# Performance work log

Measured on AMD Instinct MI355X. Metric: run time of the kernel, lower is better.

Reference implementation:

```python
import jax, jax.numpy as jnp
import numpy as np

IMAGE = 128            # canvas_size == image_size -> resize is identity
N_LINES = 32
N_SEGMENTS = 2
N_POINTS = 5           # control points per line (2 shared-endpoint quadratic beziers)
N_COLOR = 3
COORDPAIRS = np.array([[0, 1, 2], [2, 3, 4]])  # (n_segments, 3)
N_SAMPLES = 10         # polyline samples for bezier edt2 (explicit 10 in source)
POWER = 2.0            # power at progress=0 (= config.power_i)
SIGMA2 = 0.05          # annealed sigma2 at progress=0
EPS = 1e-10
BS = 4


def setup_inputs() -> dict:
    key = jax.random.key(0)
    k1, k2, k3, k4 = jax.random.split(key, 4)
    position = 0.5 * jax.random.normal(k1, (BS, N_LINES, N_POINTS * 2), jnp.float32)
    radius = jax.random.uniform(k2, (BS, N_LINES, 1), jnp.float32, minval=0.3, maxval=1.0)
    color = jax.random.uniform(k3, (BS, N_LINES, N_COLOR), jnp.float32)
    background = jax.random.uniform(k4, (BS, N_COLOR), jnp.float32)
    return {"position": position, "radius": radius, "color": color, "background": background}


def _render(position, radius, color, background):
    bs = position.shape[0]
    r = jnp.linspace(-1.0, 1.0, IMAGE)
    gy, gx = jnp.meshgrid(r, r, indexing="ij")
    grid = jnp.stack([gy, gx], axis=-1)                      # (H, W, 2)

    # --- reshape_params (background='keep', n_back=0) ---
    lines = position.reshape(bs, N_LINES, N_POINTS, 2)
    segs = lines[:, :, COORDPAIRS]                           # (bs, nl, nseg, 3, 2)
    # smooth bezier: reflect control point of segments after the first
    segs = segs.at[:, :, 1:, 1].set(2.0 * segs[:, :, 1:, 0] - segs[:, :, 1:, 1])
    curves = segs.reshape(bs, N_LINES * N_SEGMENTS, 3, 2)    # (bs, N, 3, 2)

    sigma = (radius ** 2).reshape(bs, N_LINES, 1, 1)
    sigma = jnp.repeat(sigma, N_SEGMENTS, axis=1) * SIGMA2   # (bs, N, 1, 1)
    col = jnp.repeat(color, N_SEGMENTS, axis=1)[:, :, :, None, None]  # (bs, N, nc, 1, 1)

    # --- curve_edt2_polyline: sample quadratic bezier, min segment distance ---
    t = jnp.linspace(0.0, 1.0, N_SAMPLES)
    w = jnp.stack([(1.0 - t) ** 2, 2.0 * t * (1.0 - t), t ** 2], axis=0)  # (3, T)
    pts = jnp.einsum("bnkc,kt->bntc", curves, w)             # (bs, N, T, 2)
    a, b = pts[:, :, :-1], pts[:, :, 1:]                     # (bs, N, S=T-1, 2)
    v = b - a
    v_ = v[:, :, :, None, None, :]
    d = grid[None, None, None] - a[:, :, :, None, None, :]   # (bs, N, S, H, W, 2)
    vv = jnp.sum(v * v, axis=-1)[:, :, :, None, None]
    tp = jnp.clip(jnp.sum(d * v_, axis=-1) / (vv + EPS), 0.0, 1.0)
    diff = d - tp[..., None] * v_
    edt2 = jnp.min(jnp.sum(diff * diff, axis=-1), axis=2)    # (bs, N, H, W)

    # --- intensity + rasterize + over-composite ---
    intensity = jnp.exp(-((edt2 / sigma) ** POWER))          # (bs, N, H, W)
    rasters = col * intensity[:, :, None]                    # (bs, N, nc, H, W)
    canvas = jnp.broadcast_to(background[:, None, :, None, None],
                              (bs, 1, N_COLOR, IMAGE, IMAGE))
    rasters = jnp.concatenate([rasters, canvas], axis=1)     # (bs, N+1, nc, H, W)
    inten_c = jnp.broadcast_to(intensity[:, :, None],
                               (bs, intensity.shape[1], N_COLOR, IMAGE, IMAGE))
    inten_all = jnp.concatenate([inten_c, jnp.ones_like(canvas)], axis=1)
    linv = 1.0 - inten_all + EPS
    # 'over' composite front-to-back along stroke dim: exclusive cumprod weights
    w_excl = jnp.concatenate([jnp.ones_like(linv[:, :1]),
                              jnp.cumprod(linv, axis=1)[:, :-1]], axis=1)
    images = jnp.sum(rasters * w_excl, axis=1)               # (bs, nc, H, W)
    return jnp.clip(images, 0.0, 1.0)


def reference(position, radius, color, background):
    return _render(position, radius, color, background)
```

## Files before the change

### kernel.cpp

```cpp
#include <hip/hip_runtime.h>

#define IMAGE   128
#define NLINES  32
#define NCURVE  64
#define NSUB    9
#define PIX     (IMAGE*IMAGE)

__global__ __launch_bounds__(256)
void render_kernel(const float* __restrict__ pos,
                   const float* __restrict__ rad,
                   const float* __restrict__ col,
                   const float* __restrict__ bg,
                   float* __restrict__ out)
{
    __shared__ float4 s_seg[NCURVE*NSUB];
    __shared__ float  s_rvv[NCURVE*NSUB];
    __shared__ float  s_isig[NCURVE];
    __shared__ float  s_col[NCURVE*3];
    __shared__ float  s_bg[3];

    const int tid  = threadIdx.x;
    const int b    = blockIdx.x >> 6;
    const int pblk = blockIdx.x & 63;

    for (int e = tid; e < NCURVE*NSUB; e += 256) {
        const int n    = e / NSUB;
        const int j    = e - n*NSUB;
        const int line = n >> 1;
        const int seg  = n & 1;
        const float* P = pos + (b*NLINES + line)*10;
        float c0x, c0y, c1x, c1y, c2x, c2y;
        if (seg == 0) {
            c0x = P[0]; c0y = P[1];
            c1x = P[2]; c1y = P[3];
            c2x = P[4]; c2y = P[5];
        } else {
            const float q2x = P[4], q2y = P[5];
            const float q3x = P[6], q3y = P[7];
            c0x = q2x;             c0y = q2y;
            c1x = 2.0f*q2x - q3x;  c1y = 2.0f*q2y - q3y;
            c2x = P[8];            c2y = P[9];
        }
        const float t0 = (float)j     * (1.0f/9.0f);
        const float t1 = (float)(j+1) * (1.0f/9.0f);
        float ax, ay, bx, by;
        {
            const float mt = 1.0f - t0;
            const float w0 = mt*mt, w1 = 2.0f*t0*mt, w2 = t0*t0;
            ax = w0*c0x + w1*c1x + w2*c2x;
            ay = w0*c0y + w1*c1y + w2*c2y;
        }
        {
            const float mt = 1.0f - t1;
            const float w0 = mt*mt, w1 = 2.0f*t1*mt, w2 = t1*t1;
            bx = w0*c0x + w1*c1x + w2*c2x;
            by = w0*c0y + w1*c1y + w2*c2y;
        }
        const float vx = bx - ax, vy = by - ay;
        s_seg[e] = make_float4(ax, ay, vx, vy);
        s_rvv[e] = 1.0f / (vx*vx + vy*vy + 1e-10f);
    }
    if (tid < NCURVE) {
        const float r = rad[b*NLINES + (tid >> 1)];
        s_isig[tid] = 1.0f / (r*r*0.05f);
    }
    if (tid < NCURVE*3) {
        const int n = tid/3, c = tid - n*3;
        s_col[tid] = col[(b*NLINES + (n >> 1))*3 + c];
    }
    if (tid < 3) s_bg[tid] = bg[b*3 + tid];
    __syncthreads();

    const int p = pblk*256 + tid;
    const float g0 = -1.0f + (float)(p >> 7)  * (2.0f/127.0f);
    const float g1 = -1.0f + (float)(p & 127) * (2.0f/127.0f);

    float aR = 0.0f, aG = 0.0f, aB = 0.0f, T = 1.0f;
    for (int n = 0; n < NCURVE; ++n) {
        float edt2 = 3.4e38f;
        #pragma unroll
        for (int j = 0; j < NSUB; ++j) {
            const float4 s  = s_seg[n*NSUB + j];
            const float rvv = s_rvv[n*NSUB + j];
            const float d0  = g0 - s.x;
            const float d1  = g1 - s.y;
            const float dt  = d0*s.z + d1*s.w;
            const float tp  = fminf(fmaxf(dt*rvv, 0.0f), 1.0f);
            const float e0  = d0 - tp*s.z;
            const float e1  = d1 - tp*s.w;
            edt2 = fminf(edt2, e0*e0 + e1*e1);
        }
        const float xs = edt2 * s_isig[n];
        const float I  = __expf(-xs*xs);
        const float wI = I * T;
        aR = fmaf(s_col[n*3+0], wI, aR);
        aG = fmaf(s_col[n*3+1], wI, aG);
        aB = fmaf(s_col[n*3+2], wI, aB);
        T *= (1.0f - I + 1e-10f);
    }
    aR = fmaf(s_bg[0], T, aR);
    aG = fmaf(s_bg[1], T, aG);
    aB = fmaf(s_bg[2], T, aB);

    float* o = out + b*3*PIX + p;
    o[0]     = fminf(fmaxf(aR, 0.0f), 1.0f);
    o[PIX]   = fminf(fmaxf(aG, 0.0f), 1.0f);
    o[2*PIX] = fminf(fmaxf(aB, 0.0f), 1.0f);
}

extern "C" void kernel_launch(void* const* d_in, const int* in_sizes, int n_in,
                              void* d_out, int out_size, void* d_ws, size_t ws_size,
                              hipStream_t stream) {
    const float* pos = (const float*)d_in[0];
    const float* rad = (const float*)d_in[1];
    const float* col = (const float*)d_in[2];
    const float* bg  = (const float*)d_in[3];
    float* out = (float*)d_out;

    render_kernel<<<dim3(256), dim3(256), 0, stream>>>(pos, rad, col, bg, out);
}
```

Before: 75.89 us.

## Split curve compositing across waves and precompute segment table in setup kernel

Moves the per-batch segment geometry computation into a separate single-block setup kernel that writes a padded table to workspace. The render kernel now splits the 64 curves into 8 chunks handled by different waves per 64-pixel tile, with each wave compositing its chunk and the partial (color, transmittance) results merged through shared memory using the associative over operator. This raises the launch from 256 blocks of 256 threads to 1024 blocks of 512 threads to fill the GPU. Segment data is read through wave-uniform global (scalar) loads instead of LDS. The cost is an extra kernel launch, a serial single-block setup, and a block-wide barrier followed by a reduction done by only one wave.

```diff
diff --git a/kernel.cpp b/kernel.cpp
--- a/kernel.cpp
+++ b/kernel.cpp
@@ -5,27 +5,23 @@
 #define NCURVE  64
 #define NSUB    9
 #define PIX     (IMAGE*IMAGE)
+#define BS      4
+#define NCHUNK  8
+#define CPC     8
+
+#define RECF 64
 
 __global__ __launch_bounds__(256)
-void render_kernel(const float* __restrict__ pos,
-                   const float* __restrict__ rad,
-                   const float* __restrict__ col,
-                   const float* __restrict__ bg,
-                   float* __restrict__ out)
+void setup_kernel(const float* __restrict__ pos,
+                  const float* __restrict__ rad,
+                  const float* __restrict__ col,
+                  float* __restrict__ tbl)
 {
-    __shared__ float4 s_seg[NCURVE*NSUB];
-    __shared__ float  s_rvv[NCURVE*NSUB];
-    __shared__ float  s_isig[NCURVE];
-    __shared__ float  s_col[NCURVE*3];
-    __shared__ float  s_bg[3];
-
-    const int tid  = threadIdx.x;
-    const int b    = blockIdx.x >> 6;
-    const int pblk = blockIdx.x & 63;
-
-    for (int e = tid; e < NCURVE*NSUB; e += 256) {
-        const int n    = e / NSUB;
-        const int j    = e - n*NSUB;
+    const int tid = threadIdx.x;
+    for (int e = tid; e < BS*NCURVE*NSUB; e += 256) {
+        const int j = e % NSUB;
+        const int n = (e / NSUB) & (NCURVE-1);
+        const int b = e / (NSUB*NCURVE);
         const int line = n >> 1;
         const int seg  = n & 1;
         const float* P = pos + (b*NLINES + line)*10;
@@ -57,55 +53,88 @@
             by = w0*c0y + w1*c1y + w2*c2y;
         }
         const float vx = bx - ax, vy = by - ay;
-        s_seg[e] = make_float4(ax, ay, vx, vy);
-        s_rvv[e] = 1.0f / (vx*vx + vy*vy + 1e-10f);
+        float* base = tbl + (b*NCURVE + n)*RECF;
+        base[j*4+0] = ax; base[j*4+1] = ay;
+        base[j*4+2] = vx; base[j*4+3] = vy;
+        base[36+j]  = 1.0f / (vx*vx + vy*vy + 1e-10f);
     }
-    if (tid < NCURVE) {
-        const float r = rad[b*NLINES + (tid >> 1)];
-        s_isig[tid] = 1.0f / (r*r*0.05f);
+    {
+        const int b = tid >> 6, n = tid & (NCURVE-1);
+        const int line = n >> 1;
+        const float r = rad[b*NLINES + line];
+        float* base = tbl + tid*RECF;
+        base[48] = 1.0f / (r*r*0.05f);
+        base[49] = col[(b*NLINES + line)*3 + 0];
+        base[50] = col[(b*NLINES + line)*3 + 1];
+        base[51] = col[(b*NLINES + line)*3 + 2];
     }
-    if (tid < NCURVE*3) {
-        const int n = tid/3, c = tid - n*3;
-        s_col[tid] = col[(b*NLINES + (n >> 1))*3 + c];
-    }
-    if (tid < 3) s_bg[tid] = bg[b*3 + tid];
-    __syncthreads();
+}
 
-    const int p = pblk*256 + tid;
+__global__ __launch_bounds__(512, 8)
+void render_kernel(const float* __restrict__ tbl,
+                   const float* __restrict__ bg,
+                   float* __restrict__ out)
+{
+    __shared__ float4 s_part[NCHUNK*64];
+
+    const int tid   = threadIdx.x;
+    const int b     = blockIdx.x >> 8;
+    const int tile  = blockIdx.x & 255;
+    const int px    = tid & 63;
+    const int chunk = __builtin_amdgcn_readfirstlane(tid >> 6);
+
+    const int p = tile*64 + px;
     const float g0 = -1.0f + (float)(p >> 7)  * (2.0f/127.0f);
     const float g1 = -1.0f + (float)(p & 127) * (2.0f/127.0f);
 
     float aR = 0.0f, aG = 0.0f, aB = 0.0f, T = 1.0f;
-    for (int n = 0; n < NCURVE; ++n) {
+    for (int i = 0; i < CPC; ++i) {
+        const int n = chunk*CPC + i;
+        const float* __restrict__ base = tbl + (b*NCURVE + n)*RECF;
         float edt2 = 3.4e38f;
         #pragma unroll
         for (int j = 0; j < NSUB; ++j) {
-            const float4 s  = s_seg[n*NSUB + j];
-            const float rvv = s_rvv[n*NSUB + j];
-            const float d0  = g0 - s.x;
-            const float d1  = g1 - s.y;
-            const float dt  = d0*s.z + d1*s.w;
+            const float ax = base[j*4+0], ay = base[j*4+1];
+            const float vx = base[j*4+2], vy = base[j*4+3];
+            const float rvv = base[36+j];
+            const float d0  = g0 - ax;
+            const float d1  = g1 - ay;
+            const float dt  = d0*vx + d1*vy;
             const float tp  = fminf(fmaxf(dt*rvv, 0.0f), 1.0f);
-            const float e0  = d0 - tp*s.z;
-            const float e1  = d1 - tp*s.w;
+            const float e0  = d0 - tp*vx;
+            const float e1  = d1 - tp*vy;
             edt2 = fminf(edt2, e0*e0 + e1*e1);
         }
-        const float xs = edt2 * s_isig[n];
+        const float xs = edt2 * base[48];
         const float I  = __expf(-xs*xs);
         const float wI = I * T;
-        aR = fmaf(s_col[n*3+0], wI, aR);
-        aG = fmaf(s_col[n*3+1], wI, aG);
-        aB = fmaf(s_col[n*3+2], wI, aB);
+        aR = fmaf(base[49], wI, aR);
+        aG = fmaf(base[50], wI, aG);
+        aB = fmaf(base[51], wI, aB);
         T *= (1.0f - I + 1e-10f);
     }
-    aR = fmaf(s_bg[0], T, aR);
-    aG = fmaf(s_bg[1], T, aG);
-    aB = fmaf(s_bg[2], T, aB);
+    s_part[chunk*64 + px] = make_float4(aR, aG, aB, T);
+    __syncthreads();
 
-    float* o = out + b*3*PIX + p;
-    o[0]     = fminf(fmaxf(aR, 0.0f), 1.0f);
-    o[PIX]   = fminf(fmaxf(aG, 0.0f), 1.0f);
-    o[2*PIX] = fminf(fmaxf(aB, 0.0f), 1.0f);
+    if (tid < 64) {
+        float4 acc = s_part[tid];
+        float C0 = acc.x, C1 = acc.y, C2 = acc.z, Tt = acc.w;
+        #pragma unroll
+        for (int c = 1; c < NCHUNK; ++c) {
+            const float4 q = s_part[c*64 + tid];
+            C0 = fmaf(Tt, q.x, C0);
+            C1 = fmaf(Tt, q.y, C1);
+            C2 = fmaf(Tt, q.z, C2);
+            Tt *= q.w;
+        }
+        C0 = fmaf(Tt, bg[b*3+0], C0);
+        C1 = fmaf(Tt, bg[b*3+1], C1);
+        C2 = fmaf(Tt, bg[b*3+2], C2);
+        const int po = tile*64 + tid;
+        out[(b*3+0)*PIX + po] = fminf(fmaxf(C0, 0.0f), 1.0f);
+        out[(b*3+1)*PIX + po] = fminf(fmaxf(C1, 0.0f), 1.0f);
+        out[(b*3+2)*PIX + po] = fminf(fmaxf(C2, 0.0f), 1.0f);
+    }
 }
 
 extern "C" void kernel_launch(void* const* d_in, const int* in_sizes, int n_in,
@@ -116,6 +145,8 @@
     const float* col = (const float*)d_in[2];
     const float* bg  = (const float*)d_in[3];
     float* out = (float*)d_out;
+    float* tbl = (float*)d_ws;
 
-    render_kernel<<<dim3(256), dim3(256), 0, stream>>>(pos, rad, col, bg, out);
+    setup_kernel<<<dim3(1), dim3(256), 0, stream>>>(pos, rad, col, tbl);
+    render_kernel<<<dim3(BS*256), dim3(512), 0, stream>>>(tbl, bg, out);
 }
```

New measurement: 74.12 us. 2.3% less time.
